# Kernel tuning notes

Hardware: AMD Instinct MI355X
Metric: run time of the kernel (lower is better)

The kernel has to match this reference:

```python
import jax, jax.numpy as jnp
import numpy as np

N, E, D = 10000, 160000, 512
H, C = 4, 128          # hidden layers: 4 heads x 128 = 512 (residual-compatible)
HF, CF = 2, 512        # final layer: 2 heads, concat=False (mean)
NEG_SLOPE = 0.2


def _gat(x, src, dst, W, a_src, a_dst, b, heads, out_c, concat):
    """PyG-style GATConv (v1 attention), no dropout (eval mode)."""
    n = x.shape[0]
    h = (x @ W).reshape(n, heads, out_c)                  # [N,H,C]
    es = (h * a_src).sum(-1)                              # [N,H]
    ed = (h * a_dst).sum(-1)                              # [N,H]
    e = jax.nn.leaky_relu(es[src] + ed[dst], NEG_SLOPE)   # [E,H]
    m = jax.ops.segment_max(e, dst, num_segments=n)       # softmax over in-edges of dst
    m = jnp.where(jnp.isfinite(m), m, 0.0)                # guard isolated nodes
    ex = jnp.exp(e - m[dst])
    den = jax.ops.segment_sum(ex, dst, num_segments=n)
    alpha = ex / (den[dst] + 1e-16)                       # [E,H]
    msg = h[src] * alpha[..., None]                       # [E,H,C]
    out = jax.ops.segment_sum(msg, dst, num_segments=n)   # [N,H,C]
    out = out.reshape(n, heads * out_c) if concat else out.mean(axis=1)
    return out + b


def setup_inputs() -> dict:
    key = jax.random.key(0)
    ks = jax.random.split(key, 16)
    s = 0.05
    return {
        "graph": jax.random.normal(ks[0], (N, D), jnp.float32),
        "edge_index": jax.random.randint(ks[1], (2, E), 0, N, dtype=jnp.int32),
        "W1": jax.random.normal(ks[2], (D, H * C), jnp.float32) * s,
        "as1": jax.random.normal(ks[3], (H, C), jnp.float32) * s,
        "ad1": jax.random.normal(ks[4], (H, C), jnp.float32) * s,
        "b1": jnp.zeros((H * C,), jnp.float32),
        "W2": jax.random.normal(ks[5], (H * C, H * C), jnp.float32) * s,
        "as2": jax.random.normal(ks[6], (H, C), jnp.float32) * s,
        "ad2": jax.random.normal(ks[7], (H, C), jnp.float32) * s,
        "b2": jnp.zeros((H * C,), jnp.float32),
        "W3": jax.random.normal(ks[8], (H * C, HF * CF), jnp.float32) * s,
        "as3": jax.random.normal(ks[9], (HF, CF), jnp.float32) * s,
        "ad3": jax.random.normal(ks[10], (HF, CF), jnp.float32) * s,
        "b3": jnp.zeros((CF,), jnp.float32),
    }


def reference(graph, edge_index, W1, as1, ad1, b1, W2, as2, ad2, b2, W3, as3, ad3, b3):
    src, dst = edge_index[0], edge_index[1]
    # layer_size=2: conv1 + convs[0] with ELU+residual, convs[1] (concat=False) residual only
    x = jax.nn.elu(_gat(graph, src, dst, W1, as1, ad1, b1, H, C, True) + graph)
    x = jax.nn.elu(_gat(x, src, dst, W2, as2, ad2, b2, H, C, True) + x)
    x = _gat(x, src, dst, W3, as3, ad3, b3, HF, CF, False) + x
    return x
```

## Files before the change

### kernel.cpp

```cpp
#include <hip/hip_runtime.h>
#include <hip/hip_bf16.h>
#include <hip/hip_fp16.h>
#include <cstddef>
#include <cstdint>


typedef _Float16 half8 __attribute__((ext_vector_type(8)));
typedef _Float16 half4v __attribute__((ext_vector_type(4)));
typedef float floatx4 __attribute__((ext_vector_type(4)));

#define AS1(p) ((const __attribute__((address_space(1))) void*)(p))
#define AS3(p) ((__attribute__((address_space(3))) void*)(p))

__device__ __forceinline__ float leaky_exp(float e) {
    e = (e > 0.f) ? e : 0.2f * e;
    return __expf(e);
}


__global__ void scan_kernel(const int* __restrict__ deg, int* __restrict__ row_start,
                            int* __restrict__ cursor, int n) {
    __shared__ int wsum[16];
    __shared__ int carry_s;
    int tid = threadIdx.x;
    int wave = tid >> 6, lane = tid & 63;
    if (tid == 0) { carry_s = 0; row_start[0] = 0; }
    __syncthreads();
    const int CH = 16;
    for (int base = 0; base < n; base += 1024 * CH) {
        int i0 = base + tid * CH;
        int loc[CH];
        int tsum = 0;
#pragma unroll
        for (int q = 0; q < CH; ++q) {
            int idx = i0 + q;
            int v = (idx < n) ? deg[idx] : 0;
            tsum += v;
            loc[q] = tsum;
        }
        int x = tsum;
#pragma unroll
        for (int off = 1; off < 64; off <<= 1) {
            int t = __shfl_up(x, off);
            if (lane >= off) x += t;
        }
        if (lane == 63) wsum[wave] = x;
        __syncthreads();
        if (wave == 0 && lane < 16) {
            int w = wsum[lane];
#pragma unroll
            for (int off = 1; off < 16; off <<= 1) {
                int t = __shfl_up(w, off);
                if (lane >= off) w += t;
            }
            wsum[lane] = w;
        }
        __syncthreads();
        int carry = carry_s;
        int toff = carry + (wave ? wsum[wave - 1] : 0) + (x - tsum);
#pragma unroll
        for (int q = 0; q < CH; ++q) {
            int idx = i0 + q;
            if (idx < n) {
                int excl = toff + (q ? loc[q - 1] : 0);
                row_start[idx + 1] = toff + loc[q];
                cursor[idx] = excl;
            }
        }
        __syncthreads();
        if (tid == 0) carry_s = carry + wsum[15];
        __syncthreads();
    }
}

__global__ void scatter_edges(const int* __restrict__ src, const int* __restrict__ dst,
                              int* __restrict__ cursor, int* __restrict__ srcs, int E) {
    int e = blockIdx.x * blockDim.x + threadIdx.x;
    if (e < E) {
        int p = atomicAdd(&cursor[dst[e]], 1);
        srcs[p] = src[e];
    }
}


__global__ void prep_all(const float* __restrict__ graph, _Float16* __restrict__ Ah, int n4,
                         int cb, int pb,
                         const float* __restrict__ W1, const float* __restrict__ W2,
                         const float* __restrict__ W3,
                         _Float16* __restrict__ Wt1, _Float16* __restrict__ Wt2,
                         _Float16* __restrict__ Bt3,
                         const float* __restrict__ as1, const float* __restrict__ ad1,
                         const float* __restrict__ as2, const float* __restrict__ ad2,
                         const float* __restrict__ as3, const float* __restrict__ ad3,
                         float* __restrict__ wes3, float* __restrict__ wed3,
                         const int* __restrict__ dst, int* __restrict__ deg, int E) {
    int b = blockIdx.x;
    int tid = threadIdx.x;
    if (b < cb) {
        int i = b * 256 + tid;
        if (i < n4) {
            float4 v = ((const float4*)graph)[i];
            half4v o = {(_Float16)v.x, (_Float16)v.y, (_Float16)v.z, (_Float16)v.w};
            ((half4v*)Ah)[i] = o;
        }
        return;
    }
    if (b < cb + 1024) {
        __shared__ float t[32][33];
        int bb = b - cb;
        int region = bb >> 8, idx = bb & 255;
        int r0 = (idx >> 4) * 32, c0 = (idx & 15) * 32;
        const float* in;
        _Float16* out;
        int in_ld, out_ld;
        if (region == 0)      { in = W1;       out = Wt1;       in_ld = 512;  out_ld = 512;  }
        else if (region == 1) { in = W2;       out = Wt2;       in_ld = 512;  out_ld = 512;  }
        else if (region == 2) { in = W3;       out = Bt3;       in_ld = 1024; out_ld = 1024; }
        else                  { in = W3 + 512; out = Bt3 + 512; in_ld = 1024; out_ld = 1024; }
        int tx = tid & 31, ty = tid >> 5;
        for (int i = ty; i < 32; i += 8)
            t[i][tx] = in[(size_t)(r0 + i) * in_ld + c0 + tx];
        __syncthreads();
        for (int i = ty; i < 32; i += 8)
            out[(size_t)(c0 + i) * out_ld + r0 + tx] = (_Float16)t[tx][i];
        return;
    }
    if (b >= pb) {
        int e = (b - pb) * 256 + tid;
        if (e < E) atomicAdd(&deg[dst[e]], 1);
        return;
    }
    int w = (b - cb - 1024) * 4 + (tid >> 6);
    int lane = tid & 63;
    if (w < 8192) {
        int layer = w >> 12;
        int idx = w & 4095;
        int d = idx & 511, hh = (idx >> 9) & 3, sel = idx >> 11;
        const float* W = layer ? W2 : W1;
        const float* a = layer ? (sel ? ad2 : as2) : (sel ? ad1 : as1);
        const float* row = W + (size_t)d * 512 + hh * 128;
        const float* av = a + hh * 128;
        float s = 0.f;
        s += row[lane] * av[lane];
        s += row[lane + 64] * av[lane + 64];
#pragma unroll
        for (int off = 32; off; off >>= 1) s += __shfl_down(s, off);
        if (lane == 0) {
            _Float16* Wt = layer ? Wt2 : Wt1;
            Wt[(size_t)(512 + sel * 4 + hh) * 512 + d] = (_Float16)s;
        }
    } else if (w < 10240) {
        int idx = w - 8192;
        int k = idx & 511, hh = (idx >> 9) & 1, sel = idx >> 10;
        const float* a = (sel ? ad3 : as3) + hh * 512;
        const float* row = W3 + (size_t)k * 1024 + hh * 512;
        float s = 0.f;
        for (int c = lane; c < 512; c += 64) s += row[c] * a[c];
#pragma unroll
        for (int off = 32; off; off >>= 1) s += __shfl_down(s, off);
        if (lane == 0) (sel ? wed3 : wes3)[hh * 512 + k] = s;
    } else if (w < 11136) {
        int z = (w - 10240) * 64 + lane;
        int layer = z / 28672;
        int rem = z - layer * 28672;
        int row = 520 + rem / 512, col = rem & 511;
        (layer ? Wt2 : Wt1)[(size_t)row * 512 + col] = (_Float16)0.f;
    }
}


#define BK 64

__global__ __launch_bounds__(256) void gemm_f16_att(const _Float16* __restrict__ A,
                                                    const _Float16* __restrict__ Bt,
                                                    _Float16* __restrict__ Hout,
                                                    float* __restrict__ es,
                                                    float* __restrict__ ed,
                                                    int M, int K) {
    __shared__ _Float16 As[64 * BK];
    __shared__ _Float16 Bs[64 * BK];
    int tid = threadIdx.x;
    int lane = tid & 63, wave = tid >> 6;
    int wm = (wave & 1) * 32, wn = (wave >> 1) * 32;
    int m0 = blockIdx.y * 64, n0 = blockIdx.x * 64;
    int l15 = lane & 15, quad = lane >> 4;
    int trow = tid >> 3, tcol = tid & 7;

    floatx4 acc[2][2];
#pragma unroll
    for (int i = 0; i < 2; ++i)
#pragma unroll
        for (int j = 0; j < 2; ++j) acc[i][j] = (floatx4){0.f, 0.f, 0.f, 0.f};

    for (int k0 = 0; k0 < K; k0 += BK) {
        __syncthreads();
#pragma unroll
        for (int i = 0; i < 2; ++i) {
            int gr = m0 + i * 32 + trow; if (gr >= M) gr = M - 1;
            __builtin_amdgcn_global_load_lds(AS1(A + (size_t)gr * K + k0 + tcol * 8),
                                             AS3(As + (size_t)(i * 256 + tid) * 8), 16, 0, 0);
        }
#pragma unroll
        for (int i = 0; i < 2; ++i) {
            int gr = n0 + i * 32 + trow;
            __builtin_amdgcn_global_load_lds(AS1(Bt + (size_t)gr * K + k0 + tcol * 8),
                                             AS3(Bs + (size_t)(i * 256 + tid) * 8), 16, 0, 0);
        }
        __syncthreads();
#pragma unroll
        for (int ks = 0; ks < BK; ks += 32) {
            half8 af[2], bfr[2];
#pragma unroll
            for (int i = 0; i < 2; ++i)
                af[i] = *(const half8*)&As[(wm + i * 16 + l15) * BK + ks + quad * 8];
#pragma unroll
            for (int j = 0; j < 2; ++j)
                bfr[j] = *(const half8*)&Bs[(wn + j * 16 + l15) * BK + ks + quad * 8];
#pragma unroll
            for (int i = 0; i < 2; ++i)
#pragma unroll
                for (int j = 0; j < 2; ++j)
                    acc[i][j] = __builtin_amdgcn_mfma_f32_16x16x32_f16(af[i], bfr[j], acc[i][j], 0, 0, 0);
        }
    }
#pragma unroll
    for (int i = 0; i < 2; ++i)
#pragma unroll
        for (int j = 0; j < 2; ++j) {
            int col = n0 + wn + j * 16 + l15;
#pragma unroll
            for (int r = 0; r < 4; ++r) {
                int row = m0 + wm + i * 16 + quad * 4 + r;
                if (row < M) {
                    float v = acc[i][j][r];
                    if (col < 512) Hout[(size_t)row * 512 + col] = (_Float16)v;
                    else if (col < 516) es[row * 4 + col - 512] = v;
                    else if (col < 520) ed[row * 4 + col - 516] = v;
                }
            }
        }
}

__global__ __launch_bounds__(256) void gemm_f16_ep(const _Float16* __restrict__ A,
                                                   const _Float16* __restrict__ Bt,
                                                   float* __restrict__ out,
                                                   const float* __restrict__ bias,
                                                   const _Float16* __restrict__ xres,
                                                   int M, int Nn, int K) {
    __shared__ _Float16 As[128 * BK];
    __shared__ _Float16 Bs[64 * BK];
    int tid = threadIdx.x;
    int lane = tid & 63, wave = tid >> 6;
    int wm = wave * 32;
    int m0 = blockIdx.y * 128, n0 = blockIdx.x * 64;
    int l15 = lane & 15, quad = lane >> 4;
    int trow = tid >> 3, tcol = tid & 7;

    floatx4 acc[2][4];
#pragma unroll
    for (int i = 0; i < 2; ++i)
#pragma unroll
        for (int j = 0; j < 4; ++j) acc[i][j] = (floatx4){0.f, 0.f, 0.f, 0.f};

    for (int k0 = 0; k0 < K; k0 += BK) {
        __syncthreads();
#pragma unroll
        for (int i = 0; i < 4; ++i) {
            int gr = m0 + i * 32 + trow; if (gr >= M) gr = M - 1;
            __builtin_amdgcn_global_load_lds(AS1(A + (size_t)gr * K + k0 + tcol * 8),
                                             AS3(As + (size_t)(i * 256 + tid) * 8), 16, 0, 0);
        }
#pragma unroll
        for (int i = 0; i < 2; ++i) {
            int gr = n0 + i * 32 + trow;
            __builtin_amdgcn_global_load_lds(AS1(Bt + (size_t)gr * K + k0 + tcol * 8),
                                             AS3(Bs + (size_t)(i * 256 + tid) * 8), 16, 0, 0);
        }
        __syncthreads();
#pragma unroll
        for (int ks = 0; ks < BK; ks += 32) {
            half8 af[2], bfr[4];
#pragma unroll
            for (int i = 0; i < 2; ++i)
                af[i] = *(const half8*)&As[(wm + i * 16 + l15) * BK + ks + quad * 8];
#pragma unroll
            for (int j = 0; j < 4; ++j)
                bfr[j] = *(const half8*)&Bs[(j * 16 + l15) * BK + ks + quad * 8];
#pragma unroll
            for (int i = 0; i < 2; ++i)
#pragma unroll
                for (int j = 0; j < 4; ++j)
                    acc[i][j] = __builtin_amdgcn_mfma_f32_16x16x32_f16(af[i], bfr[j], acc[i][j], 0, 0, 0);
        }
    }
#pragma unroll
    for (int i = 0; i < 2; ++i)
#pragma unroll
        for (int j = 0; j < 4; ++j) {
            int col = n0 + j * 16 + l15;
#pragma unroll
            for (int r = 0; r < 4; ++r) {
                int row = m0 + wm + i * 16 + quad * 4 + r;
                if (row < M)
                    out[(size_t)row * Nn + col] =
                        0.5f * acc[i][j][r] + bias[col] + (float)xres[(size_t)row * Nn + col];
            }
        }
}


template <bool RES32, bool COEF3>
__global__ __launch_bounds__(512) void aggregate7_concat(
    const _Float16* __restrict__ h, const float* __restrict__ es,
    const float* __restrict__ ed,
    const int* __restrict__ row_start, const int* __restrict__ srcs,
    const float* __restrict__ bias, const float* __restrict__ xres32,
    const _Float16* __restrict__ xres16, _Float16* __restrict__ x_out_h,
    const float* __restrict__ wes3, const float* __restrict__ wed3,
    float* __restrict__ es3, float* __restrict__ ed3, int Nn) {
    int wave = threadIdx.x >> 6, lane = threadIdx.x & 63;
    int n = blockIdx.x * 8 + wave;
    if (n >= Nn) return;
    int head = lane >> 4;
    int c0 = lane * 8;
    float edn = ed[n * 4 + head];
    int beg = row_start[n], end = row_start[n + 1];
    float acc[8] = {};
    float den = 0.f;
    int j = beg;
    for (; j + 3 < end; j += 4) {
        int s0 = srcs[j], s1 = srcs[j + 1], s2 = srcs[j + 2], s3 = srcs[j + 3];
        float e0 = es[s0 * 4 + head], e1 = es[s1 * 4 + head];
        float e2 = es[s2 * 4 + head], e3 = es[s3 * 4 + head];
        half8 h0 = *(const half8*)&h[(size_t)s0 * 512 + c0];
        half8 h1 = *(const half8*)&h[(size_t)s1 * 512 + c0];
        half8 h2 = *(const half8*)&h[(size_t)s2 * 512 + c0];
        half8 h3 = *(const half8*)&h[(size_t)s3 * 512 + c0];
        float w0 = leaky_exp(e0 + edn), w1 = leaky_exp(e1 + edn);
        float w2 = leaky_exp(e2 + edn), w3 = leaky_exp(e3 + edn);
        den += w0 + w1 + w2 + w3;
#pragma unroll
        for (int k = 0; k < 8; ++k) acc[k] += w0 * (float)h0[k];
#pragma unroll
        for (int k = 0; k < 8; ++k) acc[k] += w1 * (float)h1[k];
#pragma unroll
        for (int k = 0; k < 8; ++k) acc[k] += w2 * (float)h2[k];
#pragma unroll
        for (int k = 0; k < 8; ++k) acc[k] += w3 * (float)h3[k];
    }
    for (; j < end; ++j) {
        int s = srcs[j];
        float w = leaky_exp(es[s * 4 + head] + edn);
        half8 hv = *(const half8*)&h[(size_t)s * 512 + c0];
        den += w;
#pragma unroll
        for (int k = 0; k < 8; ++k) acc[k] += w * (float)hv[k];
    }
    float invden = 1.f / (den + 1e-16f);
    size_t base = (size_t)n * 512 + c0;
    float v[8];
    half8 o;
#pragma unroll
    for (int k = 0; k < 8; ++k) {
        float res = RES32 ? xres32[base + k] : (float)xres16[base + k];
        float t = acc[k] * invden + bias[c0 + k] + res;
        t = (t > 0.f) ? t : expm1f(t);
        v[k] = t;
        o[k] = (_Float16)t;
    }
    *(half8*)&x_out_h[base] = o;
    if (COEF3) {
        float t0 = 0.f, t1 = 0.f, t2 = 0.f, t3 = 0.f;
#pragma unroll
        for (int k = 0; k < 8; ++k) {
            t0 += v[k] * wes3[c0 + k];
            t1 += v[k] * wes3[512 + c0 + k];
            t2 += v[k] * wed3[c0 + k];
            t3 += v[k] * wed3[512 + c0 + k];
        }
#pragma unroll
        for (int off = 32; off; off >>= 1) {
            t0 += __shfl_down(t0, off);
            t1 += __shfl_down(t1, off);
            t2 += __shfl_down(t2, off);
            t3 += __shfl_down(t3, off);
        }
        if (lane == 0) {
            es3[n * 2] = t0; es3[n * 2 + 1] = t1;
            ed3[n * 2] = t2; ed3[n * 2 + 1] = t3;
        }
    }
}


__global__ __launch_bounds__(512) void aggregate7_dual(
    const _Float16* __restrict__ x, const float* __restrict__ es3,
    const float* __restrict__ ed3,
    const int* __restrict__ row_start, const int* __restrict__ srcs,
    _Float16* __restrict__ y, int Nn) {
    int wave = threadIdx.x >> 6, lane = threadIdx.x & 63;
    int n = blockIdx.x * 8 + wave;
    if (n >= Nn) return;
    int c0 = lane * 8;
    float edn0 = ed3[n * 2], edn1 = ed3[n * 2 + 1];
    int beg = row_start[n], end = row_start[n + 1];
    float a0[8] = {}, a1[8] = {};
    float den0 = 0.f, den1 = 0.f;
    int j = beg;
    for (; j + 3 < end; j += 4) {
        int s0 = srcs[j], s1 = srcs[j + 1], s2 = srcs[j + 2], s3 = srcs[j + 3];
        float2 q0 = *(const float2*)&es3[s0 * 2];
        float2 q1 = *(const float2*)&es3[s1 * 2];
        float2 q2 = *(const float2*)&es3[s2 * 2];
        float2 q3 = *(const float2*)&es3[s3 * 2];
        half8 h0 = *(const half8*)&x[(size_t)s0 * 512 + c0];
        half8 h1 = *(const half8*)&x[(size_t)s1 * 512 + c0];
        half8 h2 = *(const half8*)&x[(size_t)s2 * 512 + c0];
        half8 h3 = *(const half8*)&x[(size_t)s3 * 512 + c0];
        float u0 = leaky_exp(q0.x + edn0), v0 = leaky_exp(q0.y + edn1);
        float u1 = leaky_exp(q1.x + edn0), v1 = leaky_exp(q1.y + edn1);
        float u2 = leaky_exp(q2.x + edn0), v2 = leaky_exp(q2.y + edn1);
        float u3 = leaky_exp(q3.x + edn0), v3 = leaky_exp(q3.y + edn1);
        den0 += u0 + u1 + u2 + u3;
        den1 += v0 + v1 + v2 + v3;
#pragma unroll
        for (int k = 0; k < 8; ++k) { float f = (float)h0[k]; a0[k] += u0 * f; a1[k] += v0 * f; }
#pragma unroll
        for (int k = 0; k < 8; ++k) { float f = (float)h1[k]; a0[k] += u1 * f; a1[k] += v1 * f; }
#pragma unroll
        for (int k = 0; k < 8; ++k) { float f = (float)h2[k]; a0[k] += u2 * f; a1[k] += v2 * f; }
#pragma unroll
        for (int k = 0; k < 8; ++k) { float f = (float)h3[k]; a0[k] += u3 * f; a1[k] += v3 * f; }
    }
    for (; j < end; ++j) {
        int s = srcs[j];
        float2 q = *(const float2*)&es3[s * 2];
        float u = leaky_exp(q.x + edn0), v = leaky_exp(q.y + edn1);
        half8 hv = *(const half8*)&x[(size_t)s * 512 + c0];
        den0 += u; den1 += v;
#pragma unroll
        for (int k = 0; k < 8; ++k) { float f = (float)hv[k]; a0[k] += u * f; a1[k] += v * f; }
    }
    float invd0 = 1.f / (den0 + 1e-16f);
    float invd1 = 1.f / (den1 + 1e-16f);
    half8 o0, o1;
#pragma unroll
    for (int k = 0; k < 8; ++k) {
        o0[k] = (_Float16)(a0[k] * invd0);
        o1[k] = (_Float16)(a1[k] * invd1);
    }
    *(half8*)&y[(size_t)n * 1024 + c0] = o0;
    *(half8*)&y[(size_t)n * 1024 + 512 + c0] = o1;
}


extern "C" void kernel_launch(void* const* d_in, const int* in_sizes, int n_in,
                              void* d_out, int out_size, void* d_ws, size_t ws_size,
                              hipStream_t stream) {
    const float* graph = (const float*)d_in[0];
    const int* edge_index = (const int*)d_in[1];
    const float* W1 = (const float*)d_in[2];
    const float* as1 = (const float*)d_in[3];
    const float* ad1 = (const float*)d_in[4];
    const float* b1 = (const float*)d_in[5];
    const float* W2 = (const float*)d_in[6];
    const float* as2 = (const float*)d_in[7];
    const float* ad2 = (const float*)d_in[8];
    const float* b2 = (const float*)d_in[9];
    const float* W3 = (const float*)d_in[10];
    const float* as3 = (const float*)d_in[11];
    const float* ad3 = (const float*)d_in[12];
    const float* b3 = (const float*)d_in[13];

    const int D = 512;
    int N = in_sizes[0] / D;
    int E = in_sizes[1] / 2;
    const int* src = edge_index;
    const int* dst = edge_index + E;

    char* p = (char*)d_ws;
    auto carve = [&](size_t bytes) {
        void* r = (void*)p;
        p += (bytes + 255) & ~(size_t)255;
        return r;
    };
    _Float16* Ah   = (_Float16*)carve((size_t)N * 512 * 2);
    _Float16* Wt1  = (_Float16*)carve((size_t)576 * 512 * 2);
    _Float16* Wt2  = (_Float16*)carve((size_t)576 * 512 * 2);
    _Float16* Bt3  = (_Float16*)carve((size_t)512 * 1024 * 2);
    _Float16* h_h  = (_Float16*)carve((size_t)N * 1024 * 2);
    float* es      = (float*)carve((size_t)N * 4 * 4);
    float* ed      = (float*)carve((size_t)N * 4 * 4);
    float* es3     = (float*)carve((size_t)N * 2 * 4);
    float* ed3     = (float*)carve((size_t)N * 2 * 4);
    float* wes3    = (float*)carve((size_t)2 * 512 * 4);
    float* wed3    = (float*)carve((size_t)2 * 512 * 4);
    int* deg       = (int*)carve((size_t)N * 4);
    int* cur       = (int*)carve((size_t)N * 4);
    int* row_st    = (int*)carve((size_t)(N + 1) * 4);
    int* srcs      = (int*)carve((size_t)E * 4);

    hipMemsetAsync(deg, 0, (size_t)N * 4, stream);
    int n4 = N * 512 / 4;
    int cb = (n4 + 255) / 256;
    int pb = cb + 1024 + 2784;
    int eb = (E + 255) / 256;
    prep_all<<<pb + eb, 256, 0, stream>>>(
        graph, Ah, n4, cb, pb, W1, W2, W3, Wt1, Wt2, Bt3,
        as1, ad1, as2, ad2, as3, ad3, wes3, wed3, dst, deg, E);

    scan_kernel<<<1, 1024, 0, stream>>>(deg, row_st, cur, N);
    scatter_edges<<<(E + 255) / 256, 256, 0, stream>>>(src, dst, cur, srcs, E);

    int nblk8 = (N + 7) / 8;
    int mblk = (N + 63) / 64;
    int mblk128 = (N + 127) / 128;
    gemm_f16_att<<<dim3(9, mblk), 256, 0, stream>>>(Ah, Wt1, h_h, es, ed, N, 512);
    aggregate7_concat<true, false><<<nblk8, 512, 0, stream>>>(
        h_h, es, ed, row_st, srcs, b1, graph, nullptr, Ah,
        nullptr, nullptr, nullptr, nullptr, N);

    gemm_f16_att<<<dim3(9, mblk), 256, 0, stream>>>(Ah, Wt2, h_h, es, ed, N, 512);
    aggregate7_concat<false, true><<<nblk8, 512, 0, stream>>>(
        h_h, es, ed, row_st, srcs, b2, nullptr, Ah, Ah,
        wes3, wed3, es3, ed3, N);

    aggregate7_dual<<<nblk8, 512, 0, stream>>>(Ah, es3, ed3, row_st, srcs, h_h, N);
    gemm_f16_ep<<<dim3(8, mblk128), 256, 0, stream>>>(
        h_h, Bt3, (float*)d_out, b3, Ah, N, 512, 1024);
}
```

Measured before the change: 311.1 us.

## Split each node's edge list across two waves and reduce through shared memory

The aggregation kernels now give each destination node two waves instead of one. Each wave takes alternate edges, and the second wave's partial sums and denominators are combined through LDS after a block barrier. The aim is to double the memory-level parallelism per node and shorten the serial gather chain, which average degree 16 makes latency-bound. In exchange it adds shared-memory traffic, a __syncthreads, an idle half-wave during the epilogue, and twice as many blocks.

```diff
diff --git a/kernel.cpp b/kernel.cpp
--- a/kernel.cpp
+++ b/kernel.cpp
@@ -310,7 +310,7 @@
 
 
 template <bool RES32, bool COEF3>
-__global__ __launch_bounds__(512) void aggregate7_concat(
+__global__ __launch_bounds__(512) void aggregate10_concat(
     const _Float16* __restrict__ h, const float* __restrict__ es,
     const float* __restrict__ ed,
     const int* __restrict__ row_start, const int* __restrict__ srcs,
@@ -318,18 +318,22 @@
     const _Float16* __restrict__ xres16, _Float16* __restrict__ x_out_h,
     const float* __restrict__ wes3, const float* __restrict__ wed3,
     float* __restrict__ es3, float* __restrict__ ed3, int Nn) {
-    int wave = threadIdx.x >> 6, lane = threadIdx.x & 63;
-    int n = blockIdx.x * 8 + wave;
-    if (n >= Nn) return;
+    __shared__ float part[4][512];
+    __shared__ float partden[4][4];
+    int wv = threadIdx.x >> 6, lane = threadIdx.x & 63;
+    int local = wv >> 1, half = wv & 1;
+    int n = blockIdx.x * 4 + local;
+    bool active = n < Nn;
     int head = lane >> 4;
     int c0 = lane * 8;
-    float edn = ed[n * 4 + head];
-    int beg = row_start[n], end = row_start[n + 1];
+    float edn = active ? ed[n * 4 + head] : 0.f;
+    int beg = 0, end = 0;
+    if (active) { beg = row_start[n]; end = row_start[n + 1]; }
     float acc[8] = {};
     float den = 0.f;
-    int j = beg;
-    for (; j + 3 < end; j += 4) {
-        int s0 = srcs[j], s1 = srcs[j + 1], s2 = srcs[j + 2], s3 = srcs[j + 3];
+    int j = beg + half;
+    for (; j + 6 < end; j += 8) {
+        int s0 = srcs[j], s1 = srcs[j + 2], s2 = srcs[j + 4], s3 = srcs[j + 6];
         float e0 = es[s0 * 4 + head], e1 = es[s1 * 4 + head];
         float e2 = es[s2 * 4 + head], e3 = es[s3 * 4 + head];
         half8 h0 = *(const half8*)&h[(size_t)s0 * 512 + c0];
@@ -348,7 +352,7 @@
 #pragma unroll
         for (int k = 0; k < 8; ++k) acc[k] += w3 * (float)h3[k];
     }
-    for (; j < end; ++j) {
+    for (; j < end; j += 2) {
         int s = srcs[j];
         float w = leaky_exp(es[s * 4 + head] + edn);
         half8 hv = *(const half8*)&h[(size_t)s * 512 + c0];
@@ -356,59 +360,77 @@
 #pragma unroll
         for (int k = 0; k < 8; ++k) acc[k] += w * (float)hv[k];
     }
-    float invden = 1.f / (den + 1e-16f);
-    size_t base = (size_t)n * 512 + c0;
-    float v[8];
-    half8 o;
-#pragma unroll
-    for (int k = 0; k < 8; ++k) {
-        float res = RES32 ? xres32[base + k] : (float)xres16[base + k];
-        float t = acc[k] * invden + bias[c0 + k] + res;
-        t = (t > 0.f) ? t : expm1f(t);
-        v[k] = t;
-        o[k] = (_Float16)t;
-    }
-    *(half8*)&x_out_h[base] = o;
-    if (COEF3) {
-        float t0 = 0.f, t1 = 0.f, t2 = 0.f, t3 = 0.f;
+    if (half == 1) {
+#pragma unroll
+        for (int k = 0; k < 8; ++k) part[local][c0 + k] = acc[k];
+        if ((lane & 15) == 0) partden[local][head] = den;
+    }
+    __syncthreads();
+    if (half == 0 && active) {
+#pragma unroll
+        for (int k = 0; k < 8; ++k) acc[k] += part[local][c0 + k];
+        den += partden[local][head];
+        float invden = 1.f / (den + 1e-16f);
+        size_t base = (size_t)n * 512 + c0;
+        float v[8];
+        half8 o;
 #pragma unroll
         for (int k = 0; k < 8; ++k) {
-            t0 += v[k] * wes3[c0 + k];
-            t1 += v[k] * wes3[512 + c0 + k];
-            t2 += v[k] * wed3[c0 + k];
-            t3 += v[k] * wed3[512 + c0 + k];
-        }
-#pragma unroll
-        for (int off = 32; off; off >>= 1) {
-            t0 += __shfl_down(t0, off);
-            t1 += __shfl_down(t1, off);
-            t2 += __shfl_down(t2, off);
-            t3 += __shfl_down(t3, off);
-        }
-        if (lane == 0) {
-            es3[n * 2] = t0; es3[n * 2 + 1] = t1;
-            ed3[n * 2] = t2; ed3[n * 2 + 1] = t3;
-        }
-    }
-}
-
-
-__global__ __launch_bounds__(512) void aggregate7_dual(
+            float res = RES32 ? xres32[base + k] : (float)xres16[base + k];
+            float t = acc[k] * invden + bias[c0 + k] + res;
+            t = (t > 0.f) ? t : expm1f(t);
+            v[k] = t;
+            o[k] = (_Float16)t;
+        }
+        *(half8*)&x_out_h[base] = o;
+        if (COEF3) {
+            float t0 = 0.f, t1 = 0.f, t2 = 0.f, t3 = 0.f;
+#pragma unroll
+            for (int k = 0; k < 8; ++k) {
+                t0 += v[k] * wes3[c0 + k];
+                t1 += v[k] * wes3[512 + c0 + k];
+                t2 += v[k] * wed3[c0 + k];
+                t3 += v[k] * wed3[512 + c0 + k];
+            }
+#pragma unroll
+            for (int off = 32; off; off >>= 1) {
+                t0 += __shfl_down(t0, off);
+                t1 += __shfl_down(t1, off);
+                t2 += __shfl_down(t2, off);
+                t3 += __shfl_down(t3, off);
+            }
+            if (lane == 0) {
+                es3[n * 2] = t0; es3[n * 2 + 1] = t1;
+                ed3[n * 2] = t2; ed3[n * 2 + 1] = t3;
+            }
+        }
+    }
+}
+
+
+__global__ __launch_bounds__(512) void aggregate10_dual(
     const _Float16* __restrict__ x, const float* __restrict__ es3,
     const float* __restrict__ ed3,
     const int* __restrict__ row_start, const int* __restrict__ srcs,
     _Float16* __restrict__ y, int Nn) {
-    int wave = threadIdx.x >> 6, lane = threadIdx.x & 63;
-    int n = blockIdx.x * 8 + wave;
-    if (n >= Nn) return;
+    __shared__ float part[4][1024];
+    __shared__ float partden[4][2];
+    int wv = threadIdx.x >> 6, lane = threadIdx.x & 63;
+    int local = wv >> 1, half = wv & 1;
+    int n = blockIdx.x * 4 + local;
+    bool active = n < Nn;
     int c0 = lane * 8;
-    float edn0 = ed3[n * 2], edn1 = ed3[n * 2 + 1];
-    int beg = row_start[n], end = row_start[n + 1];
+    float edn0 = 0.f, edn1 = 0.f;
+    int beg = 0, end = 0;
+    if (active) {
+        edn0 = ed3[n * 2]; edn1 = ed3[n * 2 + 1];
+        beg = row_start[n]; end = row_start[n + 1];
+    }
     float a0[8] = {}, a1[8] = {};
     float den0 = 0.f, den1 = 0.f;
-    int j = beg;
-    for (; j + 3 < end; j += 4) {
-        int s0 = srcs[j], s1 = srcs[j + 1], s2 = srcs[j + 2], s3 = srcs[j + 3];
+    int j = beg + half;
+    for (; j + 6 < end; j += 8) {
+        int s0 = srcs[j], s1 = srcs[j + 2], s2 = srcs[j + 4], s3 = srcs[j + 6];
         float2 q0 = *(const float2*)&es3[s0 * 2];
         float2 q1 = *(const float2*)&es3[s1 * 2];
         float2 q2 = *(const float2*)&es3[s2 * 2];
@@ -432,7 +454,7 @@
 #pragma unroll
         for (int k = 0; k < 8; ++k) { float f = (float)h3[k]; a0[k] += u3 * f; a1[k] += v3 * f; }
     }
-    for (; j < end; ++j) {
+    for (; j < end; j += 2) {
         int s = srcs[j];
         float2 q = *(const float2*)&es3[s * 2];
         float u = leaky_exp(q.x + edn0), v = leaky_exp(q.y + edn1);
@@ -441,16 +463,34 @@
 #pragma unroll
         for (int k = 0; k < 8; ++k) { float f = (float)hv[k]; a0[k] += u * f; a1[k] += v * f; }
     }
-    float invd0 = 1.f / (den0 + 1e-16f);
-    float invd1 = 1.f / (den1 + 1e-16f);
-    half8 o0, o1;
-#pragma unroll
-    for (int k = 0; k < 8; ++k) {
-        o0[k] = (_Float16)(a0[k] * invd0);
-        o1[k] = (_Float16)(a1[k] * invd1);
-    }
-    *(half8*)&y[(size_t)n * 1024 + c0] = o0;
-    *(half8*)&y[(size_t)n * 1024 + 512 + c0] = o1;
+    if (half == 1) {
+#pragma unroll
+        for (int k = 0; k < 8; ++k) {
+            part[local][c0 + k] = a0[k];
+            part[local][512 + c0 + k] = a1[k];
+        }
+        if (lane == 0) { partden[local][0] = den0; partden[local][1] = den1; }
+    }
+    __syncthreads();
+    if (half == 0 && active) {
+#pragma unroll
+        for (int k = 0; k < 8; ++k) {
+            a0[k] += part[local][c0 + k];
+            a1[k] += part[local][512 + c0 + k];
+        }
+        den0 += partden[local][0];
+        den1 += partden[local][1];
+        float invd0 = 1.f / (den0 + 1e-16f);
+        float invd1 = 1.f / (den1 + 1e-16f);
+        half8 o0, o1;
+#pragma unroll
+        for (int k = 0; k < 8; ++k) {
+            o0[k] = (_Float16)(a0[k] * invd0);
+            o1[k] = (_Float16)(a1[k] * invd1);
+        }
+        *(half8*)&y[(size_t)n * 1024 + c0] = o0;
+        *(half8*)&y[(size_t)n * 1024 + 512 + c0] = o1;
+    }
 }
 
 
@@ -512,20 +552,20 @@
     scan_kernel<<<1, 1024, 0, stream>>>(deg, row_st, cur, N);
     scatter_edges<<<(E + 255) / 256, 256, 0, stream>>>(src, dst, cur, srcs, E);
 
-    int nblk8 = (N + 7) / 8;
+    int nblk4 = (N + 3) / 4;
     int mblk = (N + 63) / 64;
     int mblk128 = (N + 127) / 128;
     gemm_f16_att<<<dim3(9, mblk), 256, 0, stream>>>(Ah, Wt1, h_h, es, ed, N, 512);
-    aggregate7_concat<true, false><<<nblk8, 512, 0, stream>>>(
+    aggregate10_concat<true, false><<<nblk4, 512, 0, stream>>>(
         h_h, es, ed, row_st, srcs, b1, graph, nullptr, Ah,
         nullptr, nullptr, nullptr, nullptr, N);
 
     gemm_f16_att<<<dim3(9, mblk), 256, 0, stream>>>(Ah, Wt2, h_h, es, ed, N, 512);
-    aggregate7_concat<false, true><<<nblk8, 512, 0, stream>>>(
+    aggregate10_concat<false, true><<<nblk4, 512, 0, stream>>>(
         h_h, es, ed, row_st, srcs, b2, nullptr, Ah, Ah,
         wes3, wed3, es3, ed3, N);
 
-    aggregate7_dual<<<nblk8, 512, 0, stream>>>(Ah, es3, ed3, row_st, srcs, h_h, N);
+    aggregate10_dual<<<nblk4, 512, 0, stream>>>(Ah, es3, ed3, row_st, srcs, h_h, N);
     gemm_f16_ep<<<dim3(8, mblk128), 256, 0, stream>>>(
         h_h, Bt3, (float*)d_out, b3, Ah, N, 512, 1024);
 }
```

Result: faster. 303.5 us (-2.5%).
